# Kernel tuning notes

Hardware: AMD Instinct MI355X
Metric: run time of the kernel (lower is better)

## Reference

```python
import jax, jax.numpy as jnp
import numpy as np

B, L, DIM = 2, 2048, 1024
N_HEADS = 16
HEAD = DIM // N_HEADS  # 64


def setup_inputs() -> dict:
    key = jax.random.key(0)
    ks = jax.random.split(key, 7)
    s = 1.0 / np.sqrt(DIM)
    return {
        "q": jax.random.normal(ks[0], (B, L, DIM), jnp.float32),
        "k": jax.random.normal(ks[1], (B, L, DIM), jnp.float32),
        "v": jax.random.normal(ks[2], (B, L, DIM), jnp.float32),
        "Wq": jax.random.normal(ks[3], (DIM, DIM), jnp.float32) * s,
        "Wk": jax.random.normal(ks[4], (DIM, DIM), jnp.float32) * s,
        "Wv": jax.random.normal(ks[5], (DIM, DIM), jnp.float32) * s,
        "Wo": jax.random.normal(ks[6], (DIM, DIM), jnp.float32) * s,
    }


def reference(q, k, v, Wq, Wk, Wv, Wo):
    b, l, dim = q.shape
    # nn.Linear(bias=False): x @ W.T
    qp = (q @ Wq.T).reshape(b, N_HEADS, l, HEAD)  # faithful: plain view, no transpose-split
    kp = (k @ Wk.T).reshape(b, N_HEADS, l, HEAD)
    vp = (v @ Wv.T).reshape(b, N_HEADS, l, HEAD)
    attn_score = jnp.einsum('bnid,bnjd->bnij', qp, kp) / jnp.sqrt(jnp.float32(HEAD))
    attn_weight = jax.nn.softmax(attn_score, axis=3)  # dropout is identity at eval
    x = jnp.einsum('bnij,bnjd->bnid', attn_weight, vp)
    x = jnp.transpose(x, (0, 2, 1, 3)).reshape(b, l, dim)  # 'b n i d -> b i (n d)'
    return x @ Wo.T
```

## Files before the change

kernel.cpp:

```cpp
#include <hip/hip_runtime.h>
#include <hip/hip_bf16.h>

typedef __attribute__((ext_vector_type(8))) short short8;
typedef __attribute__((ext_vector_type(4))) float f32x4;
typedef __attribute__((ext_vector_type(2))) unsigned int u32x2;
typedef __attribute__((ext_vector_type(4))) unsigned int u32x4;

#define B_    2
#define L_    2048
#define DIM_  1024
#define NH_   16
#define HEAD_ 64
#define M_    4096
#define SZ_   4194304
#define WSZ_  1048576
#define SCL   0.18033688011112043f
#define MOFF  (72.0f * SCL)

#if __has_builtin(__builtin_amdgcn_exp2f)
#define EXP2(x) __builtin_amdgcn_exp2f(x)
#else
#define EXP2(x) exp2f(x)
#endif

#define BARRIER() asm volatile("s_barrier" ::: "memory")
#define VMW4()    asm volatile("s_waitcnt vmcnt(4)" ::: "memory")
#define VMW2()    asm volatile("s_waitcnt vmcnt(2)" ::: "memory")
#define VMW0()    asm volatile("s_waitcnt vmcnt(0)" ::: "memory")
#define SCHEDB()  __builtin_amdgcn_sched_barrier(0)

template<int N> struct IC { static constexpr int value = N; };

__device__ __forceinline__ unsigned short f2bf(float f) {
  __hip_bfloat16 h = __float2bfloat16(f);
  return __builtin_bit_cast(unsigned short, h);
}
__device__ __forceinline__ unsigned int pk2(float a, float b) {
  return (unsigned int)f2bf(a) | ((unsigned int)f2bf(b) << 16);
}
__device__ __forceinline__ void gl_lds16(const void* g, void* l) {
  __builtin_amdgcn_global_load_lds(
      (const __attribute__((address_space(1))) unsigned int*)g,
      (__attribute__((address_space(3))) unsigned int*)l, 16, 0, 0);
}

__device__ __forceinline__ void cvt_w_body(const float* src, unsigned short* dst, int blk) {
  const int idx = blk * 2048 + threadIdx.x * 8;
  f32x4 a = *(const f32x4*)(src + idx);
  f32x4 b = *(const f32x4*)(src + idx + 4);
  u32x4 o;
  o[0] = pk2(a[0], a[1]); o[1] = pk2(a[2], a[3]);
  o[2] = pk2(b[0], b[1]); o[3] = pk2(b[2], b[3]);
  *(u32x4*)(dst + idx) = o;
}
__device__ __forceinline__ void cvt_a_body(const float* src, unsigned short* dst, int blk) {
  const size_t i = ((size_t)blk * 256 + threadIdx.x) * 16;
  f32x4 a0 = *(const f32x4*)(src + i);
  f32x4 a1 = *(const f32x4*)(src + i + 4);
  f32x4 a2 = *(const f32x4*)(src + i + 8);
  f32x4 a3 = *(const f32x4*)(src + i + 12);
  u32x4 o0, o1;
  o0[0] = pk2(a0[0], a0[1]); o0[1] = pk2(a0[2], a0[3]);
  o0[2] = pk2(a1[0], a1[1]); o0[3] = pk2(a1[2], a1[3]);
  o1[0] = pk2(a2[0], a2[1]); o1[1] = pk2(a2[2], a2[3]);
  o1[2] = pk2(a3[0], a3[1]); o1[3] = pk2(a3[2], a3[3]);
  *(u32x4*)(dst + i)     = o0;
  *(u32x4*)(dst + i + 8) = o1;
}

__global__ __launch_bounds__(256) void cvt_all(const float* __restrict__ q,
                                               const float* __restrict__ k,
                                               const float* __restrict__ v,
                                               const float* __restrict__ w0,
                                               const float* __restrict__ w1,
                                               const float* __restrict__ w2,
                                               const float* __restrict__ w3,
                                               unsigned short* __restrict__ acts,
                                               unsigned short* __restrict__ Wb) {
  const int bid = blockIdx.x;
  if (bid < 2048) {
    const int w = bid >> 9;
    const float* src = (w == 0) ? w0 : (w == 1) ? w1 : (w == 2) ? w2 : w3;
    cvt_w_body(src, Wb + (size_t)w * WSZ_, bid & 511);
  } else {
    const int a   = (bid - 2048) >> 10;
    const int blk = (bid - 2048) & 1023;
    const float* src = (a == 0) ? q : (a == 1) ? k : v;
    cvt_a_body(src, acts + (size_t)a * SZ_, blk);
  }
}
__global__ __launch_bounds__(256) void cvt_w4(const float* __restrict__ w0,
                                              const float* __restrict__ w1,
                                              const float* __restrict__ w2,
                                              const float* __restrict__ w3,
                                              unsigned short* __restrict__ Wb) {
  const int w = blockIdx.x >> 9;
  const float* src = (w == 0) ? w0 : (w == 1) ? w1 : (w == 2) ? w2 : w3;
  cvt_w_body(src, Wb + (size_t)w * WSZ_, blockIdx.x & 511);
}
__global__ __launch_bounds__(256) void cvt_one(const float* __restrict__ src,
                                               unsigned short* __restrict__ dst) {
  cvt_a_body(src, dst, blockIdx.x);
}

template<int FINAL>
__global__ __launch_bounds__(256) void gemm_k(const unsigned short* __restrict__ Abase,
                                              size_t astride,
                                              const unsigned short* __restrict__ Wball,
                                              void* __restrict__ c0,
                                              unsigned short* __restrict__ vt,
                                              int gbase) {
  constexpr int Kdim = 1024, Ndim = 1024;
  __shared__ unsigned short Alds[2][128 * 64];
  __shared__ unsigned short Blds[2][128 * 64];
  const int t   = threadIdx.x;
  const int g   = gbase + (blockIdx.x >> 8);
  const int lin = blockIdx.x & 255;
  const int swz = (lin & 7) * 32 + (lin >> 3);
  const int m0  = (swz >> 3) * 128;
  const int n0  = (swz & 7) * 128;
  const int lane = t & 63;
  const int wid  = t >> 6;
  const int lr = lane & 15, lg = lane >> 4;
  const int wm = (wid >> 1) * 64, wn = (wid & 1) * 64;
  const int srow0 = wid * 8 + (lane >> 3);
  const int sj    = lane & 7;

  f32x4 acc[4][4] = {};

  const unsigned short* alane = Abase + (size_t)g * astride +
      (size_t)(m0 + srow0) * Kdim + (sj ^ (srow0 & 7)) * 8;
  const unsigned short* wlane = Wball + (size_t)g * WSZ_ +
      (size_t)(n0 + srow0) * Kdim + (sj ^ (srow0 & 7)) * 8;

  auto stage = [&](auto bufc) {
    constexpr int BUF = decltype(bufc)::value;
#pragma unroll
    for (int s = 0; s < 4; ++s)
      gl_lds16(alane + s * (32 * Kdim), (char*)Alds[BUF] + s * 4096 + wid * 1024);
#pragma unroll
    for (int s = 0; s < 4; ++s)
      gl_lds16(wlane + s * (32 * Kdim), (char*)Blds[BUF] + s * 4096 + wid * 1024);
    alane += 64; wlane += 64;
  };
  auto compute = [&](auto bufc) {
    constexpr int BUF = decltype(bufc)::value;
#pragma unroll
    for (int ks = 0; ks < 2; ++ks) {
      short8 af[4], bfv[4];
#pragma unroll
      for (int i = 0; i < 4; ++i) {
        const int r = wm + i * 16 + lr;
        af[i] = *(const short8*)((const char*)Alds[BUF] + r * 128 + ((ks * 64 + lg * 16) ^ ((r & 7) << 4)));
      }
#pragma unroll
      for (int j = 0; j < 4; ++j) {
        const int r = wn + j * 16 + lr;
        bfv[j] = *(const short8*)((const char*)Blds[BUF] + r * 128 + ((ks * 64 + lg * 16) ^ ((r & 7) << 4)));
      }
      __builtin_amdgcn_s_setprio(1);
#pragma unroll
      for (int i = 0; i < 4; ++i)
#pragma unroll
        for (int j = 0; j < 4; ++j)
          acc[i][j] = __builtin_amdgcn_mfma_f32_16x16x32_bf16(af[i], bfv[j], acc[i][j], 0, 0, 0);
      __builtin_amdgcn_s_setprio(0);
    }
  };

  stage(IC<0>{});
  __syncthreads();
#pragma unroll 1
  for (int it = 0; it < 8; ++it) {
    if (it * 2 + 1 < 16) stage(IC<1>{});
    compute(IC<0>{});
    __syncthreads();
    if (it * 2 + 2 < 16) stage(IC<0>{});
    compute(IC<1>{});
    __syncthreads();
  }

  const float oscale = (FINAL == 0 && g == 0) ? SCL : 1.0f;
#pragma unroll
  for (int i = 0; i < 4; ++i) {
#pragma unroll
    for (int j = 0; j < 4; ++j) {
      const int grow = m0 + wm + i * 16 + lg * 4;
      const int gcol = n0 + wn + j * 16 + lr;
      if (FINAL) {
#pragma unroll
        for (int r = 0; r < 4; ++r)
          ((float*)c0)[(size_t)(grow + r) * Ndim + gcol] = acc[i][j][r];
      } else if (g == 2) {
        const int bh_  = grow >> 7;
        const int lrow = grow & 127;
        const int ch   = lrow >> 2;
        const int dd   = gcol & 63;
        const int cc   = gcol >> 6;
        const int pos  = ((cc >> 1) & 1) * 32 + (cc >> 2) * 8 + (cc & 1) * 4;
        u32x2 pk;
        pk[0] = pk2(acc[i][j][0], acc[i][j][1]);
        pk[1] = pk2(acc[i][j][2], acc[i][j][3]);
        *(u32x2*)&vt[((size_t)((bh_ * 32 + ch) * 64 + dd)) * 64 + pos] = pk;
      } else {
        unsigned short* out = (unsigned short*)c0 + (size_t)g * SZ_;
#pragma unroll
        for (int r = 0; r < 4; ++r)
          out[(size_t)(grow + r) * Ndim + gcol] = f2bf(acc[i][j][r] * oscale);
      }
    }
  }
}

__global__ __launch_bounds__(512, 2) void attn_flash(const unsigned short* __restrict__ QKV,
                                                     const unsigned short* __restrict__ VTg,
                                                     unsigned short* __restrict__ Xout) {
  __shared__ unsigned short Klds[3][64 * 64];
  __shared__ unsigned short VTlds[3][64 * 64];

  const int t    = threadIdx.x;
  const int wv   = t >> 6;
  const int lane = t & 63;
  const int lr   = lane & 15;
  const int lg   = lane >> 4;
  const int id  = blockIdx.x;
  const int xcd = id & 7;
  const int seq = id >> 3;
  const int bh  = xcd * 4 + (seq >> 3);
  const int qt  = seq & 7;
  const int b   = bh >> 4;
  const int h   = bh & 15;
  const size_t base = (size_t)b * (L_ * DIM_) + (size_t)h * (L_ * HEAD_);
  const unsigned short* Qp = QKV + base;
  const int q0 = qt * 256;
  const int srow0 = wv * 8 + (lane >> 3);
  const int sj    = lane & 7;

  short8 qf[2][2];
#pragma unroll
  for (int u = 0; u < 2; ++u)
#pragma unroll
    for (int ks = 0; ks < 2; ++ks)
      qf[u][ks] = *(const short8*)&Qp[(size_t)(q0 + wv * 32 + u * 16 + lr) * 64 + ks * 32 + lg * 8];

  f32x4 oacc[2][4] = {};
  f32x4 lsv[2] = {};

  const unsigned short* klane = QKV + (size_t)SZ_ + base + (size_t)srow0 * 64 + (sj ^ (srow0 & 7)) * 8;
  const unsigned short* vlane = VTg + (size_t)bh * (HEAD_ * L_) + (size_t)srow0 * 64 + (sj ^ (srow0 & 7)) * 8;

  auto stage = [&](auto bufc) {
    constexpr int BUF = decltype(bufc)::value;
    gl_lds16(klane, (char*)Klds[BUF] + wv * 1024);
    gl_lds16(vlane, (char*)VTlds[BUF] + wv * 1024);
    klane += 4096; vlane += 4096;
  };
  auto chunk = [&](auto bufc) {
    constexpr int BUF = decltype(bufc)::value;
    f32x4 sacc[2][4];
#pragma unroll
    for (int u = 0; u < 2; ++u)
#pragma unroll
      for (int jf = 0; jf < 4; ++jf)
#pragma unroll
        for (int c = 0; c < 4; ++c) sacc[u][jf][c] = -MOFF;
    __builtin_amdgcn_s_setprio(1);
#pragma unroll
    for (int jf = 0; jf < 4; ++jf) {
      const int row = jf * 16 + lr;
#pragma unroll
      for (int ks = 0; ks < 2; ++ks) {
        short8 kf = *(const short8*)((const char*)Klds[BUF] + row * 128 + ((ks * 64 + lg * 16) ^ ((row & 7) << 4)));
#pragma unroll
        for (int u = 0; u < 2; ++u)
          sacc[u][jf] = __builtin_amdgcn_mfma_f32_16x16x32_bf16(kf, qf[u][ks], sacc[u][jf], 0, 0, 0);
      }
    }
    __builtin_amdgcn_s_setprio(0);
    short8 pa[2][2];
#pragma unroll
    for (int u = 0; u < 2; ++u) {
      f32x4 p[4];
#pragma unroll
      for (int jf = 0; jf < 4; ++jf)
#pragma unroll
        for (int c = 0; c < 4; ++c)
          p[jf][c] = EXP2(sacc[u][jf][c]);
      f32x4 t0, t1;
#pragma unroll
      for (int c = 0; c < 4; ++c) { t0[c] = p[0][c] + p[1][c]; t1[c] = p[2][c] + p[3][c]; }
#pragma unroll
      for (int c = 0; c < 4; ++c) lsv[u][c] += t0[c] + t1[c];
      u32x4 w0, w1;
      w0[0] = pk2(p[0][0], p[1][0]); w0[1] = pk2(p[2][0], p[3][0]);
      w0[2] = pk2(p[0][1], p[1][1]); w0[3] = pk2(p[2][1], p[3][1]);
      w1[0] = pk2(p[0][2], p[1][2]); w1[1] = pk2(p[2][2], p[3][2]);
      w1[2] = pk2(p[0][3], p[1][3]); w1[3] = pk2(p[2][3], p[3][3]);
      pa[u][0] = __builtin_bit_cast(short8, w0);
      pa[u][1] = __builtin_bit_cast(short8, w1);
    }
#pragma unroll
    for (int kk = 0; kk < 2; ++kk) {
      __builtin_amdgcn_s_setprio(1);
#pragma unroll
      for (int nf = 0; nf < 4; ++nf) {
        const int rv = nf * 16 + lr;
        short8 vf = *(const short8*)((const char*)VTlds[BUF] + rv * 128 + ((kk * 64 + lg * 16) ^ ((rv & 7) << 4)));
#pragma unroll
        for (int u = 0; u < 2; ++u)
          oacc[u][nf] = __builtin_amdgcn_mfma_f32_16x16x32_bf16(pa[u][kk], vf, oacc[u][nf], 0, 0, 0);
      }
      __builtin_amdgcn_s_setprio(0);
    }
  };

  stage(IC<0>{});
  stage(IC<1>{});
#pragma unroll 1
  for (int it = 0; it < 10; ++it) {
    stage(IC<2>{});
    SCHEDB(); VMW4(); BARRIER(); SCHEDB();
    chunk(IC<0>{});
    BARRIER();
    stage(IC<0>{});
    SCHEDB(); VMW4(); BARRIER(); SCHEDB();
    chunk(IC<1>{});
    BARRIER();
    stage(IC<1>{});
    SCHEDB(); VMW4(); BARRIER(); SCHEDB();
    chunk(IC<2>{});
    BARRIER();
  }
  SCHEDB(); VMW2(); BARRIER(); SCHEDB();
  chunk(IC<0>{});
  SCHEDB(); VMW0(); BARRIER(); SCHEDB();
  chunk(IC<1>{});

#pragma unroll
  for (int u = 0; u < 2; ++u) {
    float ls = (lsv[u][0] + lsv[u][1]) + (lsv[u][2] + lsv[u][3]);
    ls += __shfl_xor(ls, 16, 64);
    ls += __shfl_xor(ls, 32, 64);
#pragma unroll
    for (int nf = 0; nf < 4; ++nf)
#pragma unroll
      for (int c = 0; c < 4; ++c) {
        const float lq = __shfl(ls, lg * 4 + c, 64);
        const int row = q0 + wv * 32 + u * 16 + lg * 4 + c;
        Xout[(size_t)b * (L_ * DIM_) + (size_t)row * DIM_ + h * HEAD_ + nf * 16 + lr] =
            f2bf(oacc[u][nf][c] / lq);
      }
  }
}

extern "C" void kernel_launch(void* const* d_in, const int* in_sizes, int n_in,
                              void* d_out, int out_size, void* d_ws, size_t ws_size,
                              hipStream_t stream) {
  (void)in_sizes; (void)n_in; (void)out_size;
  const float* q  = (const float*)d_in[0];
  const float* k  = (const float*)d_in[1];
  const float* v  = (const float*)d_in[2];
  const float* Wq = (const float*)d_in[3];
  const float* Wk = (const float*)d_in[4];
  const float* Wv = (const float*)d_in[5];
  const float* Wo = (const float*)d_in[6];

  unsigned short* wsu = (unsigned short*)d_ws;
  const bool fused = ws_size >= (size_t)(6 * (size_t)SZ_ + 4 * (size_t)WSZ_) * 2;

  if (fused) {
    unsigned short* acts = wsu;
    unsigned short* Wb   = wsu + 3 * (size_t)SZ_;
    unsigned short* qk   = Wb + 4 * (size_t)WSZ_;
    unsigned short* vt   = qk + 2 * (size_t)SZ_;
    unsigned short* xout = acts;

    cvt_all<<<5120, 256, 0, stream>>>(q, k, v, Wq, Wk, Wv, Wo, acts, Wb);
    gemm_k<0><<<768, 256, 0, stream>>>(acts, (size_t)SZ_, Wb, qk, vt, 0);
    attn_flash<<<256, 512, 0, stream>>>(qk, vt, xout);
    gemm_k<1><<<256, 256, 0, stream>>>(xout, 0, Wb, d_out, nullptr, 3);
  } else {
    unsigned short* xab = wsu;
    unsigned short* Wb  = wsu + (size_t)SZ_;
    unsigned short* qk  = Wb + 4 * (size_t)WSZ_;
    unsigned short* vt  = qk + 2 * (size_t)SZ_;

    cvt_w4<<<2048, 256, 0, stream>>>(Wq, Wk, Wv, Wo, Wb);
    cvt_one<<<1024, 256, 0, stream>>>(q, xab);
    gemm_k<0><<<256, 256, 0, stream>>>(xab, 0, Wb, qk, vt, 0);
    cvt_one<<<1024, 256, 0, stream>>>(k, xab);
    gemm_k<0><<<256, 256, 0, stream>>>(xab, 0, Wb, qk, vt, 1);
    cvt_one<<<1024, 256, 0, stream>>>(v, xab);
    gemm_k<0><<<256, 256, 0, stream>>>(xab, 0, Wb, qk, vt, 2);
    attn_flash<<<256, 512, 0, stream>>>(qk, vt, xab);
    gemm_k<1><<<256, 256, 0, stream>>>(xab, 0, Wb, d_out, nullptr, 3);
  }
}
```

Measured before the change: 118.4 us.

## Triple-buffer GEMM LDS stages with explicit vmcnt waits for deeper prefetch

The projection GEMM moves from double to triple buffering of the A/B LDS tiles. It keeps two global-to-LDS stages in flight and uses vmcnt-counted waits plus raw barriers in place of __syncthreads. The aim is to hide more global load latency behind MFMA compute. In exchange it uses 50% more LDS per block, which may lower occupancy, and it depends on exact vmcnt accounting of the stage loads.

New measurement: 122.2 us. 1.03x slower.

```diff
diff --git a/kernel.cpp b/kernel.cpp
--- a/kernel.cpp
+++ b/kernel.cpp
@@ -24,6 +24,8 @@
 #endif
 
 #define BARRIER() asm volatile("s_barrier" ::: "memory")
+#define VMW16()   asm volatile("s_waitcnt vmcnt(16)" ::: "memory")
+#define VMW8()    asm volatile("s_waitcnt vmcnt(8)" ::: "memory")
 #define VMW4()    asm volatile("s_waitcnt vmcnt(4)" ::: "memory")
 #define VMW2()    asm volatile("s_waitcnt vmcnt(2)" ::: "memory")
 #define VMW0()    asm volatile("s_waitcnt vmcnt(0)" ::: "memory")
@@ -111,8 +113,8 @@
                                               unsigned short* __restrict__ vt,
                                               int gbase) {
   constexpr int Kdim = 1024, Ndim = 1024;
-  __shared__ unsigned short Alds[2][128 * 64];
-  __shared__ unsigned short Blds[2][128 * 64];
+  __shared__ unsigned short Alds[3][128 * 64];
+  __shared__ unsigned short Blds[3][128 * 64];
   const int t   = threadIdx.x;
   const int g   = gbase + (blockIdx.x >> 8);
   const int lin = blockIdx.x & 255;
@@ -169,16 +171,35 @@
   };
 
   stage(IC<0>{});
-  __syncthreads();
+  stage(IC<1>{});
 #pragma unroll 1
-  for (int it = 0; it < 8; ++it) {
-    if (it * 2 + 1 < 16) stage(IC<1>{});
+  for (int it = 0; it < 4; ++it) {
+    stage(IC<2>{});
+    SCHEDB(); VMW16(); BARRIER(); SCHEDB();
     compute(IC<0>{});
-    __syncthreads();
-    if (it * 2 + 2 < 16) stage(IC<0>{});
+    BARRIER();
+    stage(IC<0>{});
+    SCHEDB(); VMW16(); BARRIER(); SCHEDB();
     compute(IC<1>{});
-    __syncthreads();
-  }
+    BARRIER();
+    stage(IC<1>{});
+    SCHEDB(); VMW16(); BARRIER(); SCHEDB();
+    compute(IC<2>{});
+    BARRIER();
+  }
+  stage(IC<2>{});
+  SCHEDB(); VMW16(); BARRIER(); SCHEDB();
+  compute(IC<0>{});
+  BARRIER();
+  stage(IC<0>{});
+  SCHEDB(); VMW16(); BARRIER(); SCHEDB();
+  compute(IC<1>{});
+  BARRIER();
+  SCHEDB(); VMW8(); BARRIER(); SCHEDB();
+  compute(IC<2>{});
+  BARRIER();
+  SCHEDB(); VMW0(); BARRIER(); SCHEDB();
+  compute(IC<0>{});
 
   const float oscale = (FINAL == 0 && g == 0) ? SCL : 1.0f;
 #pragma unroll
```
